# Kernel optimization log

Measured on AMD Instinct MI355X. Metric: run time of the kernel, lower is better.

## Reference

```python
import jax, jax.numpy as jnp
import numpy as np
import math

DIMS = 2560
N_HEADS = 32
ROT_DIM = 32  # partial rotary (Phi-2)
BASE = 10000.0
B, L = 1, 2048


def apply_rope(x, rot_dim=ROT_DIM, base=BASE, offset=0):
    # x: [B, H, L, hd]; rotate first rot_dim features, pass rest through
    Lx = x.shape[2]
    D = rot_dim // 2
    pos = jnp.arange(offset, offset + Lx, dtype=jnp.float32)              # [L]
    freq = jnp.exp(-jnp.arange(D, dtype=jnp.float32) * (math.log(base) / D))  # [D]
    theta = pos[:, None] * freq[None, :]                                   # [L, D]
    cos, sin = jnp.cos(theta), jnp.sin(theta)
    x1 = x[..., :D]
    x2 = x[..., D:rot_dim]
    rx1 = x1 * cos - x2 * sin
    rx2 = x1 * sin + x2 * cos
    return jnp.concatenate([rx1, rx2, x[..., rot_dim:]], axis=-1)


def setup_inputs() -> dict:
    key = jax.random.key(0)
    k1, k2, k3, k4, k5 = jax.random.split(key, 5)
    x = jax.random.normal(k1, (B, L, DIMS), dtype=jnp.float32)
    Wqkv_w = jax.random.normal(k2, (3 * DIMS, DIMS), dtype=jnp.float32) * 0.02
    Wqkv_b = jax.random.normal(k3, (3 * DIMS,), dtype=jnp.float32) * 0.02
    out_w = jax.random.normal(k4, (DIMS, DIMS), dtype=jnp.float32) * 0.02
    out_b = jax.random.normal(k5, (DIMS,), dtype=jnp.float32) * 0.02
    # additive causal mask, broadcast over batch/heads
    mask = jnp.triu(jnp.full((L, L), -1e9, dtype=jnp.float32), k=1)[None, None]
    return {"x": x, "Wqkv_w": Wqkv_w, "Wqkv_b": Wqkv_b,
            "out_w": out_w, "out_b": out_b, "mask": mask}


def reference(x, Wqkv_w, Wqkv_b, out_w, out_b, mask):
    Bx, Lx, _ = x.shape
    hd = DIMS // N_HEADS  # 80
    qkv = x @ Wqkv_w.T + Wqkv_b                          # [B, L, 3*dims]
    q, k, v = jnp.split(qkv, 3, axis=-1)
    def to_heads(t):
        return t.reshape(Bx, Lx, N_HEADS, hd).transpose(0, 2, 1, 3)  # [B,H,L,hd]
    q, k, v = to_heads(q), to_heads(k), to_heads(v)
    q = apply_rope(q)
    k = apply_rope(k)
    scale = 1.0 / math.sqrt(hd)
    scores = scale * jnp.einsum('bhqd,bhkd->bhqk', q, k) + mask  # [B,H,L,L]
    probs = jax.nn.softmax(scores, axis=-1)
    out = jnp.einsum('bhqk,bhkd->bhqd', probs, v)
    out = out.transpose(0, 2, 1, 3).reshape(Bx, Lx, DIMS)
    return out @ out_w.T + out_b
```

## Files before the change

### kernel.cpp

```cpp
#include <hip/hip_runtime.h>
#include <cstdint>
#include <cmath>

typedef __attribute__((ext_vector_type(4))) float f32x4;
typedef __attribute__((ext_vector_type(8))) short s16x8;

#define LOG2E 1.4426950408889634f

__device__ __forceinline__ unsigned short f2bf(float f) {
    unsigned int u = __float_as_uint(f);
    u += 0x7FFFu + ((u >> 16) & 1u);
    return (unsigned short)(u >> 16);
}
__device__ __forceinline__ float bf2f(unsigned short s) {
    return __uint_as_float(((unsigned int)s) << 16);
}

__device__ __forceinline__ void async_copy16(const void* g, void* l) {
    __builtin_amdgcn_global_load_lds(
        (const __attribute__((address_space(1))) unsigned int*)(uintptr_t)g,
        (__attribute__((address_space(3))) unsigned int*)(uintptr_t)l,
        16, 0, 0);
}

__global__ __launch_bounds__(256) void cast_bf16_kernel(const float* __restrict__ in,
                                                        unsigned short* __restrict__ out,
                                                        int n4) {
    int i = blockIdx.x * 256 + threadIdx.x;
    if (i < n4) {
        float4 v = ((const float4*)in)[i];
        ushort4 o;
        o.x = f2bf(v.x); o.y = f2bf(v.y); o.z = f2bf(v.z); o.w = f2bf(v.w);
        ((ushort4*)out)[i] = o;
    }
}

template <bool BF16_OUT>
__global__ __launch_bounds__(256) void gemm_bt(const unsigned short* __restrict__ A,
                                               const unsigned short* __restrict__ B,
                                               const float* __restrict__ bias,
                                               void* __restrict__ Cout,
                                               int M, int N, int K) {
    __shared__ unsigned short As[128 * 32];
    __shared__ unsigned short Bs[128 * 32];
    const int tid  = threadIdx.x;
    const int lane = tid & 63;
    const int wv   = tid >> 6;
    const int m0 = blockIdx.y * 128;
    const int n0 = blockIdx.x * 128;
    const int w_row = (wv >> 1) * 64;
    const int w_col = (wv & 1) * 64;
    const int fr = lane & 15;
    const int fo = (lane >> 4) * 8;
    const int srow = lane >> 2;
    const int scol = (lane & 3) * 8;
    const int c0 = wv * 2;

    f32x4 acc[4][4];
    const f32x4 zf = {0.f, 0.f, 0.f, 0.f};
    for (int r = 0; r < 4; ++r)
        for (int c = 0; c < 4; ++c) acc[r][c] = zf;

    for (int k0 = 0; k0 < K; k0 += 32) {
        for (int c = c0; c < c0 + 2; ++c) {
            const unsigned short* gA = A + (size_t)(m0 + c * 16 + srow) * K + (k0 + scol);
            async_copy16(gA, &As[c * 512]);
            const unsigned short* gB = B + (size_t)(n0 + c * 16 + srow) * K + (k0 + scol);
            async_copy16(gB, &Bs[c * 512]);
        }
        __syncthreads();
        s16x8 af[4], bf[4];
        for (int r = 0; r < 4; ++r)
            af[r] = *(const s16x8*)&As[(w_row + r * 16 + fr) * 32 + fo];
        for (int c = 0; c < 4; ++c)
            bf[c] = *(const s16x8*)&Bs[(w_col + c * 16 + fr) * 32 + fo];
        for (int r = 0; r < 4; ++r)
            for (int c = 0; c < 4; ++c)
                acc[r][c] = __builtin_amdgcn_mfma_f32_16x16x32_bf16(af[r], bf[c], acc[r][c], 0, 0, 0);
        __syncthreads();
    }

    const int rb = (lane >> 4) * 4;
    for (int c = 0; c < 4; ++c) {
        int col = n0 + w_col + c * 16 + fr;
        float bv = bias[col];
        for (int r = 0; r < 4; ++r) {
            int row = m0 + w_row + r * 16 + rb;
            for (int q = 0; q < 4; ++q) {
                float v = acc[r][c][q] + bv;
                if constexpr (BF16_OUT)
                    ((unsigned short*)Cout)[(size_t)(row + q) * N + col] = f2bf(v);
                else
                    ((float*)Cout)[(size_t)(row + q) * N + col] = v;
            }
        }
    }
}

__global__ __launch_bounds__(256) void rope_kernel(unsigned short* __restrict__ qkv) {
    int g = blockIdx.x * 256 + threadIdx.x;
    int p = g >> 10;
    int i = g & 1023;
    int qk = i >> 9;
    int rem = i & 511;
    int hh = rem >> 4;
    int d = rem & 15;
    size_t base = (size_t)p * 7680 + qk * 2560 + hh * 80 + d;
    float x1 = bf2f(qkv[base]);
    float x2 = bf2f(qkv[base + 16]);
    float freq = expf(-(float)d * 0.57564627324851142f);
    float th = (float)p * freq;
    float s, c;
    sincosf(th, &s, &c);
    qkv[base]      = f2bf(x1 * c - x2 * s);
    qkv[base + 16] = f2bf(x1 * s + x2 * c);
}

__global__ __launch_bounds__(256) void pack_k_kernel(const unsigned short* __restrict__ qkv,
                                                     unsigned short* __restrict__ Kp) {
    int g = blockIdx.x * 256 + threadIdx.x;
    int c   = g % 12;
    int h   = (g / 12) & 31;
    int pos = g / 384;
    int d = c * 8;
    s16x8 v = {0, 0, 0, 0, 0, 0, 0, 0};
    if (d < 80)
        v = *(const s16x8*)(qkv + (size_t)pos * 7680 + 2560 + h * 80 + d);
    *(s16x8*)(Kp + ((size_t)h * 2048 + pos) * 96 + d) = v;
}

__global__ __launch_bounds__(256) void pack_v_kernel(const unsigned short* __restrict__ qkv,
                                                     unsigned short* __restrict__ Vp) {
    int h  = blockIdx.x & 31;
    int g64 = blockIdx.x >> 5;
    int k0 = g64 * 64;
    int tid = threadIdx.x;
    for (int ci = tid; ci < 320; ci += 256) {
        int d   = ci % 80;
        int kbl = ci / 80;
        unsigned short tmp[16];
        for (int j = 0; j < 16; ++j)
            tmp[j] = qkv[(size_t)(k0 + kbl * 16 + j) * 7680 + 5120 + h * 80 + d];
        unsigned short* dst = Vp + ((size_t)h * 128 + g64 * 4 + kbl) * 1280 + d * 16;
        *(s16x8*)dst       = *(const s16x8*)&tmp[0];
        *(s16x8*)(dst + 8) = *(const s16x8*)&tmp[8];
    }
}

__global__ __launch_bounds__(256) void flash3_kernel(const unsigned short* __restrict__ qkv,
                                                     const unsigned short* __restrict__ Kp,
                                                     const unsigned short* __restrict__ Vp,
                                                     unsigned short* __restrict__ attn) {
    __shared__ unsigned short Pt[4][640];
    __shared__ float parts[2][16][84];
    __shared__ float parts_l[2][16];
    const int tid  = threadIdx.x;
    const int lane = tid & 63;
    const int wv   = tid >> 6;
    const int h = blockIdx.x & 31;
    const int p = blockIdx.x >> 5;
    const int s    = (wv < 2) ? p : (127 - p);
    const int j    = wv & 1;
    const int slot = wv >> 1;
    const int fr = lane & 15;
    const int fg = lane >> 4;
    const float k1 = 0.11180339887498949f * LOG2E;
    const int sm16 = s * 16;

    const int n    = s + 1;
    const int half = (n + 1) >> 1;
    const int kstart = (j ? half : 0) * 16;
    const int kend   = (j ? n : half) * 16;

    s16x8 qf[3];
    {
        const unsigned short* qb = qkv + (size_t)(sm16 + fr) * 7680 + h * 80;
        const s16x8 zs = {0, 0, 0, 0, 0, 0, 0, 0};
        for (int sd = 0; sd < 3; ++sd) {
            int d = 32 * sd + fg * 8;
            qf[sd] = (d < 80) ? *(const s16x8*)(qb + d) : zs;
        }
    }

    f32x4 O[5];
    const f32x4 zf = {0.f, 0.f, 0.f, 0.f};
    for (int t = 0; t < 5; ++t) O[t] = zf;
    float rs[4] = {0.f, 0.f, 0.f, 0.f};

    const unsigned short* kptr = Kp + (size_t)h * 2048 * 96 + (size_t)(kstart + fr) * 96 + fg * 8;
    const unsigned short* vptr = Vp + (size_t)h * 128 * 1280 + (size_t)(kstart >> 4) * 1280
                                 + (fg >> 1) * 1280 + fr * 16 + (fg & 1) * 8;
    unsigned short* Pw = &Pt[wv][0];

    for (int k0 = kstart; k0 < kend; k0 += 32) {
        s16x8 kb[2][3];
        for (int g = 0; g < 2; ++g)
            for (int sd = 0; sd < 3; ++sd)
                kb[g][sd] = *(const s16x8*)(kptr + g * 1536 + sd * 32);
        s16x8 vb[5];
        for (int t = 0; t < 5; ++t)
            vb[t] = *(const s16x8*)(vptr + t * 256);

        f32x4 sa[2] = {zf, zf};
        for (int g = 0; g < 2; ++g)
            for (int sd = 0; sd < 3; ++sd)
                sa[g] = __builtin_amdgcn_mfma_f32_16x16x32_bf16(qf[sd], kb[g][sd], sa[g], 0, 0, 0);

        if (k0 + 32 > sm16 || k0 + 32 > kend) {
            for (int g = 0; g < 2; ++g)
                for (int r = 0; r < 4; ++r) {
                    int key  = k0 + g * 16 + fr;
                    int qrow = sm16 + fg * 4 + r;
                    if (key > qrow || key >= kend) sa[g][r] = -1e30f;
                }
        }

        float pr[2][4];
        for (int g = 0; g < 2; ++g)
            for (int r = 0; r < 4; ++r)
                pr[g][r] = __builtin_amdgcn_exp2f(sa[g][r] * k1);
        for (int r = 0; r < 4; ++r) rs[r] += pr[0][r] + pr[1][r];
        for (int g = 0; g < 2; ++g)
            for (int r = 0; r < 4; ++r)
                Pw[(fg * 4 + r) * 40 + g * 16 + fr] =
                    (unsigned short)(__float_as_uint(pr[g][r]) >> 16);

        s16x8 pa = *(const s16x8*)(Pw + fr * 40 + fg * 8);
        for (int t = 0; t < 5; ++t)
            O[t] = __builtin_amdgcn_mfma_f32_16x16x32_bf16(pa, vb[t], O[t], 0, 0, 0);

        kptr += 3072;
        vptr += 2560;
    }

    for (int r = 0; r < 4; ++r) {
        float v = rs[r];
        v += __shfl_xor(v, 1);
        v += __shfl_xor(v, 2);
        v += __shfl_xor(v, 4);
        v += __shfl_xor(v, 8);
        rs[r] = v;
    }

    if (j) {
        for (int t = 0; t < 5; ++t)
            for (int r = 0; r < 4; ++r)
                parts[slot][fg * 4 + r][t * 16 + fr] = O[t][r];
        if (fr == 0)
            for (int r = 0; r < 4; ++r) parts_l[slot][fg * 4 + r] = rs[r];
    }
    __syncthreads();
    if (!j) {
        for (int r = 0; r < 4; ++r) {
            float rl = 1.0f / (rs[r] + parts_l[slot][fg * 4 + r]);
            int row = sm16 + fg * 4 + r;
            for (int t = 0; t < 5; ++t) {
                float v = (O[t][r] + parts[slot][fg * 4 + r][t * 16 + fr]) * rl;
                attn[(size_t)row * 2560 + h * 80 + t * 16 + fr] = f2bf(v);
            }
        }
    }
}

extern "C" void kernel_launch(void* const* d_in, const int* in_sizes, int n_in,
                              void* d_out, int out_size, void* d_ws, size_t ws_size,
                              hipStream_t stream) {
    const float* x    = (const float*)d_in[0];
    const float* wqkv = (const float*)d_in[1];
    const float* bqkv = (const float*)d_in[2];
    const float* outw = (const float*)d_in[3];
    const float* outb = (const float*)d_in[4];

    unsigned short* xb    = (unsigned short*)d_ws;
    unsigned short* wqkvb = xb + (size_t)2048 * 2560;
    unsigned short* Kp    = wqkvb;
    unsigned short* Vp    = wqkvb + (size_t)32 * 2048 * 96;
    unsigned short* outwb = wqkvb + (size_t)7680 * 2560;
    unsigned short* qkvb  = outwb + (size_t)2560 * 2560;
    unsigned short* attnb = qkvb  + (size_t)2048 * 7680;
    float* out = (float*)d_out;

    cast_bf16_kernel<<<2048 * 2560 / 4 / 256, 256, 0, stream>>>(x, xb, 2048 * 2560 / 4);
    cast_bf16_kernel<<<7680 * 2560 / 4 / 256, 256, 0, stream>>>(wqkv, wqkvb, 7680 * 2560 / 4);
    cast_bf16_kernel<<<2560 * 2560 / 4 / 256, 256, 0, stream>>>(outw, outwb, 2560 * 2560 / 4);

    gemm_bt<true><<<dim3(7680 / 128, 2048 / 128), 256, 0, stream>>>(
        xb, wqkvb, bqkv, (void*)qkvb, 2048, 7680, 2560);

    rope_kernel<<<2048 * 1024 / 256, 256, 0, stream>>>(qkvb);

    pack_k_kernel<<<2048 * 384 / 256, 256, 0, stream>>>(qkvb, Kp);
    pack_v_kernel<<<32 * 32, 256, 0, stream>>>(qkvb, Vp);

    flash3_kernel<<<2048, 256, 0, stream>>>(qkvb, Kp, Vp, attnb);

    gemm_bt<false><<<dim3(2560 / 128, 2048 / 128), 256, 0, stream>>>(
        attnb, outwb, outb, (void*)out, 2048, 2560, 2560);
}
```

Before: 473.5 us.

## Replace block-level GEMM with single-wave 64x64 tiles and swizzled LDS

Rewrites both projection GEMMs to run one 64-thread wave per 64x64 output tile instead of four waves sharing a 128x128 tile. The change drops the __syncthreads barriers in favour of explicit waitcnt, and adds an XOR swizzle to the LDS layout to avoid bank conflicts. The aim is to remove barrier stalls and raise occupancy and grid size. In exchange, each tile is half as large, so A and B get less reuse from global memory, and loads are still not double-buffered.

```diff
diff --git a/kernel.cpp b/kernel.cpp
--- a/kernel.cpp
+++ b/kernel.cpp
@@ -36,56 +36,54 @@
 }
 
 template <bool BF16_OUT>
-__global__ __launch_bounds__(256) void gemm_bt(const unsigned short* __restrict__ A,
-                                               const unsigned short* __restrict__ B,
-                                               const float* __restrict__ bias,
-                                               void* __restrict__ Cout,
-                                               int M, int N, int K) {
-    __shared__ unsigned short As[128 * 32];
-    __shared__ unsigned short Bs[128 * 32];
-    const int tid  = threadIdx.x;
-    const int lane = tid & 63;
-    const int wv   = tid >> 6;
-    const int m0 = blockIdx.y * 128;
-    const int n0 = blockIdx.x * 128;
-    const int w_row = (wv >> 1) * 64;
-    const int w_col = (wv & 1) * 64;
+__global__ __launch_bounds__(64, 4) void gemm_wave(const unsigned short* __restrict__ A,
+                                                   const unsigned short* __restrict__ B,
+                                                   const float* __restrict__ bias,
+                                                   void* __restrict__ Cout,
+                                                   int M, int N, int K) {
+    __shared__ unsigned short As[64 * 32];
+    __shared__ unsigned short Bs[64 * 32];
+    const int lane = threadIdx.x;
+    const int m0 = blockIdx.y * 64;
+    const int n0 = blockIdx.x * 64;
     const int fr = lane & 15;
-    const int fo = (lane >> 4) * 8;
+    const int fg = lane >> 4;
     const int srow = lane >> 2;
-    const int scol = (lane & 3) * 8;
-    const int c0 = wv * 2;
+    const int scol = (((lane & 3) ^ ((lane >> 3) & 3)) * 8);
+    const int rofs = ((fg ^ ((fr >> 1) & 3)) * 8);
 
     f32x4 acc[4][4];
     const f32x4 zf = {0.f, 0.f, 0.f, 0.f};
     for (int r = 0; r < 4; ++r)
         for (int c = 0; c < 4; ++c) acc[r][c] = zf;
 
+    const unsigned short* gA = A + (size_t)(m0 + srow) * K + scol;
+    const unsigned short* gB = B + (size_t)(n0 + srow) * K + scol;
+
     for (int k0 = 0; k0 < K; k0 += 32) {
-        for (int c = c0; c < c0 + 2; ++c) {
-            const unsigned short* gA = A + (size_t)(m0 + c * 16 + srow) * K + (k0 + scol);
-            async_copy16(gA, &As[c * 512]);
-            const unsigned short* gB = B + (size_t)(n0 + c * 16 + srow) * K + (k0 + scol);
-            async_copy16(gB, &Bs[c * 512]);
-        }
-        __syncthreads();
+        asm volatile("s_waitcnt lgkmcnt(0)" ::: "memory");
+        for (int i = 0; i < 4; ++i)
+            async_copy16(gA + (size_t)i * 16 * K + k0, &As[i * 512]);
+        for (int i = 0; i < 4; ++i)
+            async_copy16(gB + (size_t)i * 16 * K + k0, &Bs[i * 512]);
+        asm volatile("s_waitcnt vmcnt(0)" ::: "memory");
+
         s16x8 af[4], bf[4];
         for (int r = 0; r < 4; ++r)
-            af[r] = *(const s16x8*)&As[(w_row + r * 16 + fr) * 32 + fo];
+            af[r] = *(const s16x8*)&As[(r * 16 + fr) * 32 + rofs];
         for (int c = 0; c < 4; ++c)
-            bf[c] = *(const s16x8*)&Bs[(w_col + c * 16 + fr) * 32 + fo];
+            bf[c] = *(const s16x8*)&Bs[(c * 16 + fr) * 32 + rofs];
         for (int r = 0; r < 4; ++r)
             for (int c = 0; c < 4; ++c)
                 acc[r][c] = __builtin_amdgcn_mfma_f32_16x16x32_bf16(af[r], bf[c], acc[r][c], 0, 0, 0);
-        __syncthreads();
-    }
-
-    const int rb = (lane >> 4) * 4;
+    }
+
+    const int rb = fg * 4;
     for (int c = 0; c < 4; ++c) {
-        int col = n0 + w_col + c * 16 + fr;
+        int col = n0 + c * 16 + fr;
         float bv = bias[col];
         for (int r = 0; r < 4; ++r) {
-            int row = m0 + w_row + r * 16 + rb;
+            int row = m0 + r * 16 + rb;
             for (int q = 0; q < 4; ++q) {
                 float v = acc[r][c][q] + bv;
                 if constexpr (BF16_OUT)
@@ -284,7 +282,7 @@
     cast_bf16_kernel<<<7680 * 2560 / 4 / 256, 256, 0, stream>>>(wqkv, wqkvb, 7680 * 2560 / 4);
     cast_bf16_kernel<<<2560 * 2560 / 4 / 256, 256, 0, stream>>>(outw, outwb, 2560 * 2560 / 4);
 
-    gemm_bt<true><<<dim3(7680 / 128, 2048 / 128), 256, 0, stream>>>(
+    gemm_wave<true><<<dim3(7680 / 64, 2048 / 64), 64, 0, stream>>>(
         xb, wqkvb, bqkv, (void*)qkvb, 2048, 7680, 2560);
 
     rope_kernel<<<2048 * 1024 / 256, 256, 0, stream>>>(qkvb);
@@ -294,6 +292,6 @@
 
     flash3_kernel<<<2048, 256, 0, stream>>>(qkvb, Kp, Vp, attnb);
 
-    gemm_bt<false><<<dim3(2560 / 128, 2048 / 128), 256, 0, stream>>>(
+    gemm_wave<false><<<dim3(2560 / 64, 2048 / 64), 64, 0, stream>>>(
         attnb, outwb, outb, (void*)out, 2048, 2560, 2560);
 }
```

Measured after the change: 499.6 us. 5.5% more time.
